# Performance work log

Measured on AMD Instinct MI355X. Metric: run time of the kernel, lower is better.

## Reference

```python
import jax, jax.numpy as jnp
import numpy as np

B, N, OUTERDIM, DIM, N_CLASSES = 2, 6000, 1024, 512, 2
HEADS, DIM_HEAD, INNER = 8, 64, 512
LANDMARKS, PINV_ITERS, KPAD = 256, 6, 16  # residual conv kernel 33 -> pad 16
SCALE = DIM_HEAD ** -0.5


def layer_norm(x, g, b, eps=1e-5):
    mu = x.mean(-1, keepdims=True)
    var = jnp.var(x, axis=-1, keepdims=True)
    return (x - mu) * jax.lax.rsqrt(var + eps) * g + b


def moore_penrose_pinv(x, iters=PINV_ITERS):
    # x: [b, h, m, m]
    abs_x = jnp.abs(x)
    col = abs_x.sum(-1)
    row = abs_x.sum(-2)
    z = jnp.swapaxes(x, -1, -2) / (jnp.max(col) * jnp.max(row))
    I = jnp.eye(x.shape[-1], dtype=x.dtype)
    for _ in range(iters):
        xz = x @ z
        z = 0.25 * z @ (13 * I - xz @ (15 * I - xz @ (7 * I - xz)))
    return z


def nystrom_attention(x, w_qkv, w_out, b_out, conv_w):
    b, n, _ = x.shape
    pad = (-n) % LANDMARKS
    xp = jnp.pad(x, ((0, 0), (pad, 0), (0, 0)))  # pad at FRONT, as in lucidrains impl
    npad = n + pad
    qkv = xp @ w_qkv.T  # [b, npad, 3*inner]
    q, k, v = [t.reshape(b, npad, HEADS, DIM_HEAD).transpose(0, 2, 1, 3)
               for t in jnp.split(qkv, 3, axis=-1)]
    q = q * SCALE
    l = npad // LANDMARKS  # tokens per landmark
    q_l = q.reshape(b, HEADS, LANDMARKS, l, DIM_HEAD).sum(3) / l
    k_l = k.reshape(b, HEADS, LANDMARKS, l, DIM_HEAD).sum(3) / l
    attn1 = jax.nn.softmax(jnp.einsum('bhid,bhjd->bhij', q, k_l), axis=-1)   # [b,h,npad,m]
    attn2 = jax.nn.softmax(jnp.einsum('bhid,bhjd->bhij', q_l, k_l), axis=-1)  # [b,h,m,m]
    attn3 = jax.nn.softmax(jnp.einsum('bhid,bhjd->bhij', q_l, k), axis=-1)    # [b,h,m,npad]
    out = (attn1 @ moore_penrose_pinv(attn2)) @ (attn3 @ v)  # [b,h,npad,d]
    # depthwise residual conv over sequence dim (per head), kernel (33,1)
    out = out + jax.lax.conv_general_dilated(
        v, conv_w, window_strides=(1, 1), padding=((KPAD, KPAD), (0, 0)),
        dimension_numbers=('NCHW', 'OIHW', 'NCHW'), feature_group_count=HEADS)
    out = out.transpose(0, 2, 1, 3).reshape(b, npad, INNER)
    out = out @ w_out.T + b_out
    return out[:, -n:]


def setup_inputs() -> dict:
    key = jax.random.key(0)
    ks = jax.random.split(key, 12)
    w = lambda k, shape: 0.02 * jax.random.normal(k, shape, dtype=jnp.float32)
    inp = {
        'data': jax.random.normal(ks[0], (B, N, OUTERDIM), dtype=jnp.float32),
        'w1': w(ks[1], (DIM, OUTERDIM)), 'b1': jnp.zeros((DIM,), jnp.float32),
        'cls_token': jax.random.normal(ks[2], (1, 1, DIM), dtype=jnp.float32),
        'ln1_g': jnp.ones((DIM,), jnp.float32), 'ln1_b': jnp.zeros((DIM,), jnp.float32),
        'qkv1_w': w(ks[3], (3 * INNER, DIM)),
        'out1_w': w(ks[4], (DIM, INNER)), 'out1_b': jnp.zeros((DIM,), jnp.float32),
        'conv1_w': w(ks[5], (HEADS, 1, 33, 1)),
        'ln2_g': jnp.ones((DIM,), jnp.float32), 'ln2_b': jnp.zeros((DIM,), jnp.float32),
        'qkv2_w': w(ks[6], (3 * INNER, DIM)),
        'out2_w': w(ks[7], (DIM, INNER)), 'out2_b': jnp.zeros((DIM,), jnp.float32),
        'conv2_w': w(ks[8], (HEADS, 1, 33, 1)),
        'lnf_g': jnp.ones((DIM,), jnp.float32), 'lnf_b': jnp.zeros((DIM,), jnp.float32),
        'w2': w(ks[9], (N_CLASSES, DIM)), 'b2': jnp.zeros((N_CLASSES,), jnp.float32),
    }
    return inp


def reference(data, w1, b1, cls_token, ln1_g, ln1_b, qkv1_w, out1_w, out1_b, conv1_w,
              ln2_g, ln2_b, qkv2_w, out2_w, out2_b, conv2_w, lnf_g, lnf_b, w2, b2):
    h = jax.nn.relu(data @ w1.T + b1)  # [B, N, DIM]
    H = h.shape[1]
    side = int(np.ceil(np.sqrt(H)))
    add = side * side - H
    h = jnp.concatenate([h, h[:, :add]], axis=1)  # square padding: 6084
    cls = jnp.broadcast_to(cls_token, (h.shape[0], 1, h.shape[2]))
    h = jnp.concatenate([cls, h], axis=1)  # +CLS: 6085
    h = h + nystrom_attention(layer_norm(h, ln1_g, ln1_b), qkv1_w, out1_w, out1_b, conv1_w)
    h = h + nystrom_attention(layer_norm(h, ln2_g, ln2_b), qkv2_w, out2_w, out2_b, conv2_w)
    h = layer_norm(h, lnf_g, lnf_b)[:, 0]
    logits = h @ w2.T + b2
    return logits
```

## Files before the change

### kernel.cpp

```cpp
#include <hip/hip_runtime.h>
#include <cstdint>
#include <cstddef>

namespace {

constexpr int DIMC  = 512;
constexpr int SEQ   = 6085;
constexpr int NPAD  = 6144;
constexpr int PADF  = 59;
constexpr int LMK   = 256;
constexpr int BHN   = 16;
constexpr int KSPL  = 16;
constexpr int MPADR = 6016;

typedef __attribute__((ext_vector_type(8))) short bf8_t;
typedef __attribute__((ext_vector_type(4))) float f4_t;

#define MFMA(a, b, c) __builtin_amdgcn_mfma_f32_16x16x32_bf16(a, b, c, 0, 0, 0)

#define SWZB(r, cu) (((((r) << 6) + ((cu) << 1))) ^ (((r) & 7) << 4))

#define GLDS16(gp, lp) __builtin_amdgcn_global_load_lds( \
    (const __attribute__((address_space(1))) void*)(gp), \
    (__attribute__((address_space(3))) void*)(lp), 16, 0, 0)

__device__ __forceinline__ ushort f2bf(float f) {
    union { float f; uint32_t u; } c{f};
    uint32_t u = c.u;
    return (ushort)((u + 0x7FFFu + ((u >> 16) & 1u)) >> 16);
}
__device__ __forceinline__ float bf2f(ushort u) {
    union { uint32_t u; float f; } c{(uint32_t)u << 16};
    return c.f;
}

__device__ __forceinline__ float waveSum(float v) {
#pragma unroll
    for (int o = 32; o > 0; o >>= 1) v += __shfl_xor(v, o, 64);
    return v;
}
__device__ __forceinline__ float waveMax(float v) {
#pragma unroll
    for (int o = 32; o > 0; o >>= 1) v = fmaxf(v, __shfl_xor(v, o, 64));
    return v;
}
__device__ __forceinline__ float blockSum256(float v, float* sm) {
    v = waveSum(v);
    __syncthreads();
    if ((threadIdx.x & 63) == 0) sm[threadIdx.x >> 6] = v;
    __syncthreads();
    return sm[0] + sm[1] + sm[2] + sm[3];
}
__device__ __forceinline__ float blockMax256(float v, float* sm) {
    v = waveMax(v);
    __syncthreads();
    if ((threadIdx.x & 63) == 0) sm[threadIdx.x >> 6] = v;
    __syncthreads();
    return fmaxf(fmaxf(sm[0], sm[1]), fmaxf(sm[2], sm[3]));
}
__device__ __forceinline__ float grpMax(float v) {
    v = fmaxf(v, __shfl_xor(v, 1, 64));
    v = fmaxf(v, __shfl_xor(v, 2, 64));
    v = fmaxf(v, __shfl_xor(v, 4, 64));
    v = fmaxf(v, __shfl_xor(v, 8, 64));
    return v;
}
__device__ __forceinline__ float grpSum(float v) {
    v += __shfl_xor(v, 1, 64);
    v += __shfl_xor(v, 2, 64);
    v += __shfl_xor(v, 4, 64);
    v += __shfl_xor(v, 8, 64);
    return v;
}

template<int EPI>
__global__ __launch_bounds__(256)
void gemm_bt(const ushort* __restrict__ A, const ushort* __restrict__ B,
             void* __restrict__ Cv, int M, int N, int K,
             int lda, int ldb, int ldc,
             long long sA, long long sB, long long sC,
             const float* __restrict__ bias, int relu,
             ushort* __restrict__ qp, ushort* __restrict__ kp, ushort* __restrict__ vp)
{
    __shared__ __align__(16) char As_s[128 * 128];
    __shared__ __align__(16) char Bs_s[128 * 128];
    const int z = blockIdx.z;
    const ushort* Ab = A + (size_t)z * sA;
    const ushort* Bb = B + (size_t)z * sB;
    const int row0 = blockIdx.y * 128, col0 = blockIdx.x * 128;
    const int tid = threadIdx.x, wid = tid >> 6, lane = tid & 63;
    const int wr = wid >> 1, wc = wid & 1, lr = lane & 15, kg = lane >> 4;
    const int srow = lane >> 3, sq = lane & 7;
    f4_t acc[4][4] = {};
    for (int k0 = 0; k0 < K; k0 += 64) {
        __syncthreads();
#pragma unroll
        for (int i = 0; i < 4; ++i) {
            int r = wid * 32 + i * 8 + srow;
            int qs = sq ^ (r & 7);
            GLDS16(Ab + (size_t)(row0 + r) * lda + k0 + qs * 8,
                   As_s + (wid * 32 + i * 8) * 128);
        }
#pragma unroll
        for (int i = 0; i < 4; ++i) {
            int r = wid * 32 + i * 8 + srow;
            int qs = sq ^ (r & 7);
            GLDS16(Bb + (size_t)(col0 + r) * ldb + k0 + qs * 8,
                   Bs_s + (wid * 32 + i * 8) * 128);
        }
        asm volatile("s_waitcnt vmcnt(0)" ::: "memory");
        __syncthreads();
#pragma unroll
        for (int ks = 0; ks < 2; ++ks) {
            bf8_t af[4], bg[4];
#pragma unroll
            for (int mr = 0; mr < 4; ++mr) {
                int r = wr * 64 + mr * 16 + lr;
                af[mr] = *(const bf8_t*)(As_s + r * 128 + ((((ks << 2) | kg) ^ (r & 7)) << 4));
            }
#pragma unroll
            for (int nr = 0; nr < 4; ++nr) {
                int r = wc * 64 + nr * 16 + lr;
                bg[nr] = *(const bf8_t*)(Bs_s + r * 128 + ((((ks << 2) | kg) ^ (r & 7)) << 4));
            }
#pragma unroll
            for (int mr = 0; mr < 4; ++mr)
#pragma unroll
                for (int nr = 0; nr < 4; ++nr)
                    acc[mr][nr] = MFMA(af[mr], bg[nr], acc[mr][nr]);
        }
    }
#pragma unroll
    for (int mr = 0; mr < 4; ++mr) {
#pragma unroll
        for (int nr = 0; nr < 4; ++nr) {
#pragma unroll
            for (int r = 0; r < 4; ++r) {
                int gm = row0 + wr * 64 + mr * 16 + kg * 4 + r;
                int gn = col0 + wc * 64 + nr * 16 + lr;
                if (gm >= M || gn >= N) continue;
                float val = acc[mr][nr][r];
                if (EPI == 0) {
                    if (bias) val += bias[gn];
                    if (relu) val = fmaxf(val, 0.f);
                    ((float*)Cv)[(size_t)z * sC + (size_t)gm * ldc + gn] = val;
                } else if (EPI == 1) {
                    ((ushort*)Cv)[(size_t)z * sC + (size_t)gm * ldc + gn] = f2bf(val);
                } else {
                    int b = (gm >= NPAD) ? 1 : 0;
                    int i = gm - b * NPAD;
                    int which = gn >> 9, hh = (gn >> 6) & 7, d = gn & 63;
                    if (which == 0)
                        qp[((size_t)(b * 8 + hh) * NPAD + i) * 64 + d] = f2bf(val * 0.125f);
                    else if (which == 1)
                        kp[((size_t)(b * 8 + hh) * NPAD + i) * 64 + d] = f2bf(val);
                    else
                        vp[((size_t)(b * 8 + hh) * 64 + d) * NPAD + i] = f2bf(val);
                }
            }
        }
    }
}

__global__ __launch_bounds__(256)
void pv_flash(const ushort* __restrict__ ql, const ushort* __restrict__ k,
              const ushort* __restrict__ vT, float* __restrict__ o2p,
              float* __restrict__ lmb, float* __restrict__ lsb)
{
    __shared__ __align__(16) char P_s[128 * 256];
    const int split = blockIdx.x, mt = blockIdx.y, bh = blockIdx.z;
    const int tid = threadIdx.x, wid = tid >> 6, lane = tid & 63;
    const int lr = lane & 15, kg = lane >> 4;
    const int rowb = wid * 32;
    const ushort* qlb = ql + ((size_t)bh * LMK + mt * 128) * 64;
    const ushort* kb  = k  + (size_t)bh * NPAD * 64;
    const ushort* vTb = vT + (size_t)bh * 64 * NPAD;
    const int kv0 = split * (NPAD / KSPL);

    float mrun[2][4], lrun[2][4];
    f4_t acco[2][4] = {};
#pragma unroll
    for (int mf = 0; mf < 2; ++mf)
#pragma unroll
        for (int r = 0; r < 4; ++r) { mrun[mf][r] = -3.0e38f; lrun[mf][r] = 0.f; }

    for (int kvt = 0; kvt < 3; ++kvt) {
        const int kvb = kv0 + kvt * 128;
        f4_t sacc[2][8] = {};
#pragma unroll
        for (int ks = 0; ks < 2; ++ks) {
            bf8_t af[2];
#pragma unroll
            for (int mf = 0; mf < 2; ++mf)
                af[mf] = *(const bf8_t*)&qlb[(size_t)(rowb + mf * 16 + lr) * 64 + ks * 32 + kg * 8];
#pragma unroll
            for (int nf = 0; nf < 8; ++nf) {
                bf8_t bg = *(const bf8_t*)&kb[(size_t)(kvb + nf * 16 + lr) * 64 + ks * 32 + kg * 8];
                sacc[0][nf] = MFMA(af[0], bg, sacc[0][nf]);
                sacc[1][nf] = MFMA(af[1], bg, sacc[1][nf]);
            }
        }
#pragma unroll
        for (int mf = 0; mf < 2; ++mf) {
            float tmax[4] = {-3.0e38f, -3.0e38f, -3.0e38f, -3.0e38f};
#pragma unroll
            for (int nf = 0; nf < 8; ++nf)
#pragma unroll
                for (int r = 0; r < 4; ++r) tmax[r] = fmaxf(tmax[r], sacc[mf][nf][r]);
#pragma unroll
            for (int r = 0; r < 4; ++r) {
                tmax[r] = grpMax(tmax[r]);
                float mnew = fmaxf(mrun[mf][r], tmax[r]);
                float sc = __expf(mrun[mf][r] - mnew);
                mrun[mf][r] = mnew;
                lrun[mf][r] *= sc;
#pragma unroll
                for (int nf2 = 0; nf2 < 4; ++nf2) acco[mf][nf2][r] *= sc;
            }
            float lsum[4] = {0.f, 0.f, 0.f, 0.f};
            const int rb2 = rowb + mf * 16 + kg * 4;
            const int cc2 = (lr & 7) * 2, chi = lr >> 3;
#pragma unroll
            for (int nf = 0; nf < 8; ++nf)
#pragma unroll
                for (int r = 0; r < 4; ++r) {
                    float e = __expf(sacc[mf][nf][r] - mrun[mf][r]);
                    lsum[r] += e;
                    int row = rb2 + r;
                    int chunk = (2 * nf + chi) ^ (row & 7);
                    *(ushort*)(P_s + row * 256 + chunk * 16 + cc2) = f2bf(e);
                }
#pragma unroll
            for (int r = 0; r < 4; ++r) lrun[mf][r] += grpSum(lsum[r]);
        }
#pragma unroll
        for (int kt2 = 0; kt2 < 4; ++kt2) {
            bf8_t af2[2];
#pragma unroll
            for (int mf = 0; mf < 2; ++mf) {
                int row = rowb + mf * 16 + lr;
                int chunk = (kt2 * 4 + kg) ^ (row & 7);
                af2[mf] = *(const bf8_t*)(P_s + row * 256 + chunk * 16);
            }
#pragma unroll
            for (int nf2 = 0; nf2 < 4; ++nf2) {
                bf8_t bg = *(const bf8_t*)&vTb[(size_t)(nf2 * 16 + lr) * NPAD + kvb + kt2 * 32 + kg * 8];
                acco[0][nf2] = MFMA(af2[0], bg, acco[0][nf2]);
                acco[1][nf2] = MFMA(af2[1], bg, acco[1][nf2]);
            }
        }
    }
#pragma unroll
    for (int mf = 0; mf < 2; ++mf)
#pragma unroll
        for (int nf2 = 0; nf2 < 4; ++nf2)
#pragma unroll
            for (int r = 0; r < 4; ++r) {
                int gm = mt * 128 + rowb + mf * 16 + kg * 4 + r;
                o2p[((size_t)(split * BHN + bh) * LMK + gm) * 64 + nf2 * 16 + lr] = acco[mf][nf2][r];
            }
    if (lr == 0) {
#pragma unroll
        for (int mf = 0; mf < 2; ++mf)
#pragma unroll
            for (int r = 0; r < 4; ++r) {
                int gm = mt * 128 + rowb + mf * 16 + kg * 4 + r;
                lmb[(size_t)(split * BHN + bh) * LMK + gm] = mrun[mf][r];
                lsb[(size_t)(split * BHN + bh) * LMK + gm] = lrun[mf][r];
            }
    }
}

__global__ void reduce_o2(const float* __restrict__ o2p, const float* __restrict__ lmb,
                          const float* __restrict__ lsb, ushort* __restrict__ o2)
{
    int idx = blockIdx.x * 256 + threadIdx.x;
    int bh = idx >> 14, m = (idx >> 6) & 255, d = idx & 63;
    float gm = -3.0e38f;
#pragma unroll
    for (int s = 0; s < KSPL; ++s)
        gm = fmaxf(gm, lmb[(size_t)(s * BHN + bh) * LMK + m]);
    float num = 0.f, den = 0.f;
#pragma unroll
    for (int s = 0; s < KSPL; ++s) {
        float wgt = __expf(lmb[(size_t)(s * BHN + bh) * LMK + m] - gm);
        num += wgt * o2p[((size_t)(s * BHN + bh) * LMK + m) * 64 + d];
        den += wgt * lsb[(size_t)(s * BHN + bh) * LMK + m];
    }
    o2[idx] = f2bf(num / den);
}

__global__ __launch_bounds__(256)
void attn1_fused(const ushort* __restrict__ q, const ushort* __restrict__ kl,
                 const ushort* __restrict__ Wt, ushort* __restrict__ ot)
{
    __shared__ __align__(16) char P_s[64 * 512];
    const int mt = blockIdx.x;
    const int bh = blockIdx.y;
    const int b = bh >> 3, hh = bh & 7;
    const int tid = threadIdx.x, wid = tid >> 6, lane = tid & 63;
    const int lr = lane & 15, kg = lane >> 4;
    const int row0 = mt * 64, rowb = wid * 16;
    const ushort* qb  = q  + (size_t)bh * NPAD * 64;
    const ushort* klb = kl + (size_t)bh * LMK * 64;
    const ushort* Wtb = Wt + (size_t)bh * 128 * 256;

    f4_t acc[16];
#pragma unroll
    for (int nf = 0; nf < 16; ++nf) acc[nf] = (f4_t){0.f, 0.f, 0.f, 0.f};
#pragma unroll
    for (int ks = 0; ks < 2; ++ks) {
        bf8_t af = *(const bf8_t*)&qb[(size_t)(row0 + rowb + lr) * 64 + ks * 32 + kg * 8];
#pragma unroll
        for (int nf = 0; nf < 16; ++nf) {
            bf8_t bg = *(const bf8_t*)&klb[(size_t)(nf * 16 + lr) * 64 + ks * 32 + kg * 8];
            acc[nf] = MFMA(af, bg, acc[nf]);
        }
    }
    float inv_s[4];
    {
        float mx[4] = {-3.0e38f, -3.0e38f, -3.0e38f, -3.0e38f};
#pragma unroll
        for (int nf = 0; nf < 16; ++nf)
#pragma unroll
            for (int r = 0; r < 4; ++r) mx[r] = fmaxf(mx[r], acc[nf][r]);
#pragma unroll
        for (int r = 0; r < 4; ++r) mx[r] = grpMax(mx[r]);
        float sum[4] = {0.f, 0.f, 0.f, 0.f};
        const int rb2 = rowb + kg * 4;
        const int cc2 = (lr & 7) * 2, chi = lr >> 3;
#pragma unroll
        for (int nf = 0; nf < 16; ++nf)
#pragma unroll
            for (int r = 0; r < 4; ++r) {
                float e = __expf(acc[nf][r] - mx[r]);
                sum[r] += e;
                int row = rb2 + r;
                int chunk = (2 * nf + chi) ^ (row & 7);
                *(ushort*)(P_s + row * 512 + chunk * 16 + cc2) = f2bf(e);
            }
#pragma unroll
        for (int r = 0; r < 4; ++r) inv_s[r] = 1.f / grpSum(sum[r]);
    }
    f4_t acc2[4] = {};
#pragma unroll
    for (int kt = 0; kt < 8; ++kt) {
        int row = rowb + lr;
        int chunk = (kt * 4 + kg) ^ (row & 7);
        bf8_t af2 = *(const bf8_t*)(P_s + row * 512 + chunk * 16);
#pragma unroll
        for (int nf = 0; nf < 4; ++nf) {
            bf8_t bg = *(const bf8_t*)&Wtb[(size_t)(nf * 16 + lr) * 256 + kt * 32 + kg * 8];
            acc2[nf] = MFMA(af2, bg, acc2[nf]);
        }
    }
#pragma unroll
    for (int nf = 0; nf < 4; ++nf)
#pragma unroll
        for (int r = 0; r < 4; ++r) {
            int gm = row0 + rowb + kg * 4 + r;
            int gn = nf * 16 + lr;
            ot[((size_t)(b * NPAD + gm)) * DIMC + hh * 64 + gn] = f2bf(acc2[nf][r] * inv_s[r]);
        }
}

__global__ __launch_bounds__(256)
void gemm_ns(const ushort* __restrict__ A, const ushort* __restrict__ B,
             ushort* __restrict__ C, ushort* __restrict__ C2, ushort* __restrict__ CT,
             float alpha, float c2d, int K, int N,
             long long sA, long long sB, long long sC, long long sCT)
{
    __shared__ __align__(16) char As_s[64 * 64];
    __shared__ __align__(16) char Bs_s[64 * 64];
    const int z = blockIdx.z;
    const int row0 = blockIdx.y * 64, col0 = blockIdx.x * 64;
    const int tid = threadIdx.x;
    const int wid = tid >> 6, lane = tid & 63;
    const int lr = lane & 15, kg = lane >> 4;
    const ushort* Ab = A + (size_t)z * sA;
    const ushort* Bb = B + (size_t)z * sB;
    f4_t acc[4] = {};
    const int am = tid >> 2, ac8 = (tid & 3) * 8;
    for (int k0 = 0; k0 < K; k0 += 32) {
        *(bf8_t*)(As_s + SWZB(am, ac8)) = *(const bf8_t*)&Ab[(size_t)(row0 + am) * K + k0 + ac8];
#pragma unroll
        for (int p = 0; p < 8; ++p) {
            int kk = p * 4 + (tid >> 6), n = tid & 63;
            *(ushort*)(Bs_s + SWZB(n, kk)) = Bb[(size_t)(k0 + kk) * N + col0 + n];
        }
        __syncthreads();
        bf8_t af = *(const bf8_t*)(As_s + SWZB(wid * 16 + lr, kg * 8));
#pragma unroll
        for (int j = 0; j < 4; ++j) {
            bf8_t bg = *(const bf8_t*)(Bs_s + SWZB(j * 16 + lr, kg * 8));
            acc[j] = MFMA(af, bg, acc[j]);
        }
        __syncthreads();
    }
#pragma unroll
    for (int j = 0; j < 4; ++j) {
#pragma unroll
        for (int r = 0; r < 4; ++r) {
            int gm = row0 + wid * 16 + kg * 4 + r;
            int gn = col0 + j * 16 + lr;
            float val = alpha * acc[j][r];
            if (C)  C[(size_t)z * sC + (size_t)gm * N + gn] = f2bf(val);
            if (C2) C2[(size_t)z * sC + (size_t)gm * N + gn] = f2bf(((gm == gn) ? c2d : 0.f) - val);
            if (CT) CT[(size_t)z * sCT + (size_t)gn * LMK + gm] = f2bf(val);
        }
    }
}

__global__ void cvt_bf16(const float* __restrict__ in, ushort* __restrict__ out, int n8) {
    int i = blockIdx.x * 256 + threadIdx.x;
    if (i >= n8) return;
    float4 a = ((const float4*)in)[i * 2], b = ((const float4*)in)[i * 2 + 1];
    ushort4 lo = { f2bf(a.x), f2bf(a.y), f2bf(a.z), f2bf(a.w) };
    ushort4 hi = { f2bf(b.x), f2bf(b.y), f2bf(b.z), f2bf(b.w) };
    ((ushort4*)out)[i * 2] = lo;
    ((ushort4*)out)[i * 2 + 1] = hi;
}

__global__ void extend_h(float* __restrict__ h, const float* __restrict__ cls) {
    int b = blockIdx.y, bx = blockIdx.x;
    float* hb = h + (size_t)b * SEQ * DIMC;
    for (int c = threadIdx.x; c < DIMC; c += 256) {
        if (bx == 0) hb[c] = cls[c];
        else hb[(size_t)(6000 + bx) * DIMC + c] = hb[(size_t)bx * DIMC + c];
    }
}

__global__ void zero_xp_pad(ushort* __restrict__ xp) {
    int e = blockIdx.x * 256 + threadIdx.x;
    int b = e / (PADF * DIMC);
    int rest = e - b * (PADF * DIMC);
    xp[(size_t)b * NPAD * DIMC + rest] = 0;
}

__global__ __launch_bounds__(128)
void ln_to_xp(const float* __restrict__ h, const float* __restrict__ g,
              const float* __restrict__ bb, ushort* __restrict__ xp)
{
    __shared__ float sm[2];
    int r = blockIdx.x;
    int b = r / SEQ, i = r - b * SEQ;
    int t = threadIdx.x;
    const float4* row = (const float4*)(h + (size_t)r * DIMC);
    float4 x = row[t];
    float s  = x.x + x.y + x.z + x.w;
    float sq = x.x * x.x + x.y * x.y + x.z * x.z + x.w * x.w;
    s = waveSum(s);
    sq = waveSum(sq);
    int w = t >> 6;
    if ((t & 63) == 0) sm[w] = s;
    __syncthreads();
    float S = sm[0] + sm[1];
    __syncthreads();
    if ((t & 63) == 0) sm[w] = sq;
    __syncthreads();
    float SQ = sm[0] + sm[1];
    float mu = S * (1.f / DIMC);
    float var = SQ * (1.f / DIMC) - mu * mu;
    float rs = rsqrtf(var + 1e-5f);
    float4 gg = ((const float4*)g)[t];
    float4 bv = ((const float4*)bb)[t];
    ushort4 o;
    o.x = f2bf((x.x - mu) * rs * gg.x + bv.x);
    o.y = f2bf((x.y - mu) * rs * gg.y + bv.y);
    o.z = f2bf((x.z - mu) * rs * gg.z + bv.z);
    o.w = f2bf((x.w - mu) * rs * gg.w + bv.w);
    ((ushort4*)(xp + ((size_t)b * NPAD + PADF + i) * DIMC))[t] = o;
}

__global__ void landmark_mean(const ushort* __restrict__ in, ushort* __restrict__ out) {
    int m = blockIdx.x, bh = blockIdx.y, d = threadIdx.x;
    const ushort* p = in + ((size_t)bh * NPAD + (size_t)m * (NPAD / LMK)) * 64 + d;
    float s = 0.f;
#pragma unroll
    for (int j = 0; j < NPAD / LMK; ++j) s += bf2f(p[(size_t)j * 64]);
    out[((size_t)bh * LMK + m) * 64 + d] = f2bf(s * (1.f / (NPAD / LMK)));
}

__global__ __launch_bounds__(256)
void softmax_bf256(ushort* __restrict__ S) {
    __shared__ float sm[4];
    ushort* p = S + (size_t)blockIdx.x * 256;
    int t = threadIdx.x;
    float v = bf2f(p[t]);
    float bm = blockMax256(v, sm);
    float e = __expf(v - bm);
    float bs = blockSum256(e, sm);
    p[t] = f2bf(e / bs);
}

__global__ __launch_bounds__(256)
void colsum_max(const ushort* __restrict__ X, float* __restrict__ scal) {
    __shared__ float sm[4];
    int bh = blockIdx.x, t = threadIdx.x;
    const ushort* Xb = X + ((size_t)bh << 16);
    float s = 0.f;
#pragma unroll 8
    for (int i = 0; i < 256; ++i) s += bf2f(Xb[(size_t)i * 256 + t]);
    float m = blockMax256(s, sm);
    if (t == 0) atomicMax((unsigned int*)scal, __float_as_uint(m));
}

__global__ void init_z(const ushort* __restrict__ X, const float* __restrict__ scal,
                       ushort* __restrict__ Z) {
    size_t e = (size_t)blockIdx.x * 256 + threadIdx.x;
    int c = (int)(e & 255);
    int r = (int)((e >> 8) & 255);
    size_t bh = e >> 16;
    float inv = 1.f / scal[0];
    Z[e] = f2bf(bf2f(X[(bh << 16) + (size_t)c * 256 + r]) * inv);
}

__global__ __launch_bounds__(256)
void conv_add(const ushort* __restrict__ vT, const float* __restrict__ cw,
              ushort* __restrict__ ot)
{
    __shared__ float w[33];
    __shared__ ushort vt[64][97];
    int bh = blockIdx.y;
    int b = bh >> 3, hh = bh & 7;
    int i0 = blockIdx.x * 64;
    int t = threadIdx.x;
    if (t < 33) w[t] = cw[hh * 33 + t];
    const ushort* vTb = vT + (size_t)bh * 64 * NPAD;
    for (int idx = t; idx < 64 * 96; idx += 256) {
        int d = idx / 96, jj = idx - d * 96;
        int j = i0 - 16 + jj;
        vt[d][jj] = (j >= 0 && j < NPAD) ? vTb[(size_t)d * NPAD + j] : (ushort)0;
    }
    __syncthreads();
    int d = t & 63;
    for (int ii = t >> 6; ii < 64; ii += 4) {
        float acc = 0.f;
#pragma unroll
        for (int kk = 0; kk < 33; ++kk) acc += w[kk] * bf2f(vt[d][ii + kk]);
        size_t off = ((size_t)(b * NPAD + i0 + ii)) * DIMC + hh * 64 + d;
        ot[off] = f2bf(bf2f(ot[off]) + acc);
    }
}

__global__ void residual_add(float* __restrict__ h, const float* __restrict__ y) {
    size_t e = (size_t)blockIdx.x * 256 + threadIdx.x;
    int c = (int)(e & 511);
    size_t ri = e >> 9;
    int i = (int)(ri % SEQ);
    int b = (int)(ri / SEQ);
    h[e] += y[((size_t)b * NPAD + PADF + i) * DIMC + c];
}

__global__ __launch_bounds__(256)
void final_head(const float* __restrict__ h, const float* __restrict__ g,
                const float* __restrict__ bb, const float* __restrict__ w2,
                const float* __restrict__ b2, float* __restrict__ out)
{
    __shared__ float row[DIMC];
    __shared__ float sm[4];
    int b = blockIdx.x;
    int t = threadIdx.x;
    const float* x = h + (size_t)b * SEQ * DIMC;
    float v0 = x[t], v1 = x[t + 256];
    float S = blockSum256(v0 + v1, sm);
    float SQ = blockSum256(v0 * v0 + v1 * v1, sm);
    float mu = S * (1.f / DIMC);
    float rs = rsqrtf(SQ * (1.f / DIMC) - mu * mu + 1e-5f);
    row[t] = (v0 - mu) * rs * g[t] + bb[t];
    row[t + 256] = (v1 - mu) * rs * g[t + 256] + bb[t + 256];
    __syncthreads();
    if (t < 64) {
        float a0 = 0.f, a1 = 0.f;
        for (int idx = t; idx < DIMC; idx += 64) {
            a0 += row[idx] * w2[idx];
            a1 += row[idx] * w2[DIMC + idx];
        }
        a0 = waveSum(a0);
        a1 = waveSum(a1);
        if (t == 0) {
            out[b * 2 + 0] = a0 + b2[0];
            out[b * 2 + 1] = a1 + b2[1];
        }
    }
}

void bt(int epi, const ushort* A, const ushort* B, void* C, int M, int N, int K,
        int lda, int ldb, int ldc, long long sA, long long sB, long long sC, int batch,
        const float* bias, int relu, ushort* qp, ushort* kp, ushort* vp, hipStream_t s)
{
    dim3 g((N + 127) / 128, (M + 127) / 128, batch), blk(256);
    switch (epi) {
    case 0: gemm_bt<0><<<g, blk, 0, s>>>(A, B, C, M, N, K, lda, ldb, ldc, sA, sB, sC, bias, relu, qp, kp, vp); break;
    case 1: gemm_bt<1><<<g, blk, 0, s>>>(A, B, C, M, N, K, lda, ldb, ldc, sA, sB, sC, bias, relu, qp, kp, vp); break;
    default: gemm_bt<2><<<g, blk, 0, s>>>(A, B, C, M, N, K, lda, ldb, ldc, sA, sB, sC, bias, relu, qp, kp, vp); break;
    }
}

void ns(const ushort* A, const ushort* B, ushort* C, ushort* C2, ushort* CT,
        float alpha, float c2d, int M, int N, int K,
        long long sA, long long sB, long long sC, long long sCT, hipStream_t s)
{
    dim3 g(N / 64, M / 64, BHN), blk(256);
    gemm_ns<<<g, blk, 0, s>>>(A, B, C, C2, CT, alpha, c2d, K, N, sA, sB, sC, sCT);
}

struct WS {
    float *h, *scal, *o2p, *y, *lmb, *lsb;
    ushort *xp, *q, *k, *vT, *ql, *kl;
    ushort *datab, *w1b, *qkvwb1, *qkvwb2, *outwb1, *outwb2;
    ushort *X, *Z0, *Z1, *XZ, *TA, *TB, *TC;
    ushort *o2b, *Wt, *S, *ot;
};

void nystrom_layer(float* h, const float* lng, const float* lnb,
                   const ushort* qkvwb, const ushort* outwb, const float* outb,
                   const float* convw, const WS& w, hipStream_t s)
{
    const long long SM = (long long)LMK * LMK;
    zero_xp_pad<<<(2 * PADF * DIMC) / 256, 256, 0, s>>>(w.xp);
    ln_to_xp<<<2 * SEQ, 128, 0, s>>>(h, lng, lnb, w.xp);
    bt(2, w.xp, qkvwb, nullptr, 2 * NPAD, 3 * DIMC, DIMC, DIMC, DIMC, 0,
       0, 0, 0, 1, nullptr, 0, w.q, w.k, w.vT, s);
    landmark_mean<<<dim3(LMK, BHN), 64, 0, s>>>(w.q, w.ql);
    landmark_mean<<<dim3(LMK, BHN), 64, 0, s>>>(w.k, w.kl);
    bt(1, w.ql, w.kl, w.X, LMK, LMK, 64, 64, 64, LMK,
       (long long)LMK * 64, (long long)LMK * 64, SM, BHN, nullptr, 0, nullptr, nullptr, nullptr, s);
    softmax_bf256<<<BHN * LMK, 256, 0, s>>>(w.X);
    hipMemsetAsync(w.scal, 0, 8, s);
    colsum_max<<<BHN, 256, 0, s>>>(w.X, w.scal);
    init_z<<<(BHN * LMK * LMK) / 256, 256, 0, s>>>(w.X, w.scal, w.Z0);
    ushort* Zc = w.Z0;
    ushort* Zn = w.Z1;
    for (int it = 0; it < 6; ++it) {
        ns(w.X, Zc, w.XZ, w.TA, nullptr, 1.f, 7.f, LMK, LMK, LMK, SM, SM, SM, 0, s);
        ns(w.XZ, w.TA, w.TB, w.TC, nullptr, 1.f, 15.f, LMK, LMK, LMK, SM, SM, SM, 0, s);
        ns(w.XZ, w.TC, w.TB, w.TA, nullptr, 1.f, 13.f, LMK, LMK, LMK, SM, SM, SM, 0, s);
        ns(Zc, w.TA, Zn, nullptr, nullptr, 0.25f, 0.f, LMK, LMK, LMK, SM, SM, SM, 0, s);
        ushort* t = Zc; Zc = Zn; Zn = t;
    }
    pv_flash<<<dim3(KSPL, 2, BHN), 256, 0, s>>>(w.ql, w.k, w.vT, w.o2p, w.lmb, w.lsb);
    reduce_o2<<<BHN * LMK * 64 / 256, 256, 0, s>>>(w.o2p, w.lmb, w.lsb, w.o2b);
    ns(Zc, w.o2b, nullptr, nullptr, w.Wt, 1.f, 0.f, LMK, 64, LMK,
       SM, (long long)LMK * 64, 0, 128 * 256, s);
    attn1_fused<<<dim3(NPAD / 64, BHN), 256, 0, s>>>(w.q, w.kl, w.Wt, w.ot);
    conv_add<<<dim3(NPAD / 64, BHN), 256, 0, s>>>(w.vT, convw, w.ot);
    bt(0, w.ot, outwb, w.y, 2 * NPAD, DIMC, DIMC, DIMC, DIMC, DIMC,
       0, 0, 0, 1, outb, 0, nullptr, nullptr, nullptr, s);
    residual_add<<<(2 * SEQ * DIMC) / 256, 256, 0, s>>>(h, w.y);
}

}

extern "C" void kernel_launch(void* const* d_in, const int* in_sizes, int n_in,
                              void* d_out, int out_size, void* d_ws, size_t ws_size,
                              hipStream_t stream)
{
    (void)in_sizes; (void)n_in; (void)out_size;
    const float* data  = (const float*)d_in[0];
    const float* w1    = (const float*)d_in[1];
    const float* b1    = (const float*)d_in[2];
    const float* cls   = (const float*)d_in[3];
    const float* ln1g  = (const float*)d_in[4];
    const float* ln1b  = (const float*)d_in[5];
    const float* qkv1w = (const float*)d_in[6];
    const float* out1w = (const float*)d_in[7];
    const float* out1b = (const float*)d_in[8];
    const float* conv1 = (const float*)d_in[9];
    const float* ln2g  = (const float*)d_in[10];
    const float* ln2b  = (const float*)d_in[11];
    const float* qkv2w = (const float*)d_in[12];
    const float* out2w = (const float*)d_in[13];
    const float* out2b = (const float*)d_in[14];
    const float* conv2 = (const float*)d_in[15];
    const float* lnfg  = (const float*)d_in[16];
    const float* lnfb  = (const float*)d_in[17];
    const float* w2    = (const float*)d_in[18];
    const float* b2    = (const float*)d_in[19];
    float* out = (float*)d_out;

    if (ws_size < 209473792ull) return;
    char* p = (char*)d_ws;
    auto alloc = [&](size_t bytes) { char* r = p; p += (bytes + 255) & ~(size_t)255; return r; };
    WS w;
    w.h     = (float*)alloc((size_t)2 * SEQ * DIMC * 4);
    w.xp    = (ushort*)alloc((size_t)2 * NPAD * DIMC * 2);
    w.q     = (ushort*)alloc((size_t)BHN * NPAD * 64 * 2);
    w.k     = (ushort*)alloc((size_t)BHN * NPAD * 64 * 2);
    w.vT    = (ushort*)alloc((size_t)BHN * 64 * NPAD * 2);
    w.ql    = (ushort*)alloc((size_t)BHN * LMK * 64 * 2);
    w.kl    = (ushort*)alloc((size_t)BHN * LMK * 64 * 2);
    w.scal  = (float*)alloc(256);
    w.datab = (ushort*)alloc((size_t)2 * MPADR * 1024 * 2);
    w.w1b   = (ushort*)alloc((size_t)512 * 1024 * 2);
    w.qkvwb1= (ushort*)alloc((size_t)1536 * 512 * 2);
    w.qkvwb2= (ushort*)alloc((size_t)1536 * 512 * 2);
    w.outwb1= (ushort*)alloc((size_t)512 * 512 * 2);
    w.outwb2= (ushort*)alloc((size_t)512 * 512 * 2);
    w.X     = (ushort*)alloc((size_t)BHN * LMK * LMK * 2);
    w.Z0    = (ushort*)alloc((size_t)BHN * LMK * LMK * 2);
    w.Z1    = (ushort*)alloc((size_t)BHN * LMK * LMK * 2);
    w.XZ    = (ushort*)alloc((size_t)BHN * LMK * LMK * 2);
    w.TA    = (ushort*)alloc((size_t)BHN * LMK * LMK * 2);
    w.TB    = (ushort*)alloc((size_t)BHN * LMK * LMK * 2);
    w.TC    = (ushort*)alloc((size_t)BHN * LMK * LMK * 2);
    w.o2p   = (float*)alloc((size_t)KSPL * BHN * LMK * 64 * 4);
    w.lmb   = (float*)alloc((size_t)KSPL * BHN * LMK * 4);
    w.lsb   = (float*)alloc((size_t)KSPL * BHN * LMK * 4);
    w.o2b   = (ushort*)alloc((size_t)BHN * LMK * 64 * 2);
    w.Wt    = (ushort*)alloc((size_t)BHN * 128 * 256 * 2);
    w.S     = (ushort*)alloc((size_t)BHN * LMK * NPAD * 2);
    w.y     = (float*)w.S;
    w.ot    = w.k;

    for (int b = 0; b < 2; ++b)
        cvt_bf16<<<3000, 256, 0, stream>>>(data + (size_t)b * 6000 * 1024,
                                           w.datab + (size_t)b * MPADR * 1024, 768000);
    cvt_bf16<<<256, 256, 0, stream>>>(w1, w.w1b, 65536);
    cvt_bf16<<<384, 256, 0, stream>>>(qkv1w, w.qkvwb1, 98304);
    cvt_bf16<<<384, 256, 0, stream>>>(qkv2w, w.qkvwb2, 98304);
    cvt_bf16<<<128, 256, 0, stream>>>(out1w, w.outwb1, 32768);
    cvt_bf16<<<128, 256, 0, stream>>>(out2w, w.outwb2, 32768);

    bt(0, w.datab, w.w1b, w.h + DIMC, 6000, DIMC, 1024, 1024, 1024, DIMC,
       (long long)MPADR * 1024, 0, (long long)SEQ * DIMC, 2, b1, 1,
       nullptr, nullptr, nullptr, stream);
    extend_h<<<dim3(85, 2), 256, 0, stream>>>(w.h, cls);

    nystrom_layer(w.h, ln1g, ln1b, w.qkvwb1, w.outwb1, out1b, conv1, w, stream);
    nystrom_layer(w.h, ln2g, ln2b, w.qkvwb2, w.outwb2, out2b, conv2, w, stream);

    final_head<<<2, 256, 0, stream>>>(w.h, lnfg, lnfb, w2, b2, out);
}
```

Measured before the change: 1.094 ms.

## Fuse residual depthwise conv into attn1 kernel and widen pv_flash split count

Removes the separate conv_add kernel: the QKV GEMM epilogue now also writes V in row-major layout, and attn1_fused stages a 96-row V window in shared memory and adds the 33-tap depthwise conv before its bf16 store. This avoids re-reading and re-writing the attention output. pv_flash now processes a single 128-token KV tile per block (KSPL raised to 48) with no online rescaling, giving more parallel blocks, while reduce_o2 merges three times as many partials. The extra V copy adds a write in the GEMM epilogue, and the y buffer is aliased onto the enlarged o2p buffer.

Result: slower. 1.131 ms (+3.4%).

```diff
diff --git a/kernel.cpp b/kernel.cpp
--- a/kernel.cpp
+++ b/kernel.cpp
@@ -10,7 +10,7 @@
 constexpr int PADF  = 59;
 constexpr int LMK   = 256;
 constexpr int BHN   = 16;
-constexpr int KSPL  = 16;
+constexpr int KSPL  = 48;
 constexpr int MPADR = 6016;
 
 typedef __attribute__((ext_vector_type(8))) short bf8_t;
@@ -80,7 +80,8 @@
              int lda, int ldb, int ldc,
              long long sA, long long sB, long long sC,
              const float* __restrict__ bias, int relu,
-             ushort* __restrict__ qp, ushort* __restrict__ kp, ushort* __restrict__ vp)
+             ushort* __restrict__ qp, ushort* __restrict__ kp,
+             ushort* __restrict__ vp, ushort* __restrict__ vtp)
 {
     __shared__ __align__(16) char As_s[128 * 128];
     __shared__ __align__(16) char Bs_s[128 * 128];
@@ -150,12 +151,16 @@
                     int b = (gm >= NPAD) ? 1 : 0;
                     int i = gm - b * NPAD;
                     int which = gn >> 9, hh = (gn >> 6) & 7, d = gn & 63;
+                    int bh = b * 8 + hh;
                     if (which == 0)
-                        qp[((size_t)(b * 8 + hh) * NPAD + i) * 64 + d] = f2bf(val * 0.125f);
+                        qp[((size_t)bh * NPAD + i) * 64 + d] = f2bf(val * 0.125f);
                     else if (which == 1)
-                        kp[((size_t)(b * 8 + hh) * NPAD + i) * 64 + d] = f2bf(val);
-                    else
-                        vp[((size_t)(b * 8 + hh) * 64 + d) * NPAD + i] = f2bf(val);
+                        kp[((size_t)bh * NPAD + i) * 64 + d] = f2bf(val);
+                    else {
+                        ushort bv = f2bf(val);
+                        vp[((size_t)bh * NPAD + i) * 64 + d] = bv;
+                        vtp[((size_t)bh * 64 + d) * NPAD + i] = bv;
+                    }
                 }
             }
         }
@@ -175,79 +180,63 @@
     const ushort* qlb = ql + ((size_t)bh * LMK + mt * 128) * 64;
     const ushort* kb  = k  + (size_t)bh * NPAD * 64;
     const ushort* vTb = vT + (size_t)bh * 64 * NPAD;
-    const int kv0 = split * (NPAD / KSPL);
-
-    float mrun[2][4], lrun[2][4];
+    const int kvb = split * 128;
+
+    f4_t sacc[2][8] = {};
+#pragma unroll
+    for (int ks = 0; ks < 2; ++ks) {
+        bf8_t af[2];
+#pragma unroll
+        for (int mf = 0; mf < 2; ++mf)
+            af[mf] = *(const bf8_t*)&qlb[(size_t)(rowb + mf * 16 + lr) * 64 + ks * 32 + kg * 8];
+#pragma unroll
+        for (int nf = 0; nf < 8; ++nf) {
+            bf8_t bg = *(const bf8_t*)&kb[(size_t)(kvb + nf * 16 + lr) * 64 + ks * 32 + kg * 8];
+            sacc[0][nf] = MFMA(af[0], bg, sacc[0][nf]);
+            sacc[1][nf] = MFMA(af[1], bg, sacc[1][nf]);
+        }
+    }
+    float mloc[2][4], lloc[2][4];
+#pragma unroll
+    for (int mf = 0; mf < 2; ++mf) {
+        float tmax[4] = {-3.0e38f, -3.0e38f, -3.0e38f, -3.0e38f};
+#pragma unroll
+        for (int nf = 0; nf < 8; ++nf)
+#pragma unroll
+            for (int r = 0; r < 4; ++r) tmax[r] = fmaxf(tmax[r], sacc[mf][nf][r]);
+#pragma unroll
+        for (int r = 0; r < 4; ++r) { tmax[r] = grpMax(tmax[r]); mloc[mf][r] = tmax[r]; }
+        float lsum[4] = {0.f, 0.f, 0.f, 0.f};
+        const int rb2 = rowb + mf * 16 + kg * 4;
+        const int cc2 = (lr & 7) * 2, chi = lr >> 3;
+#pragma unroll
+        for (int nf = 0; nf < 8; ++nf)
+#pragma unroll
+            for (int r = 0; r < 4; ++r) {
+                float e = __expf(sacc[mf][nf][r] - tmax[r]);
+                lsum[r] += e;
+                int row = rb2 + r;
+                int chunk = (2 * nf + chi) ^ (row & 7);
+                *(ushort*)(P_s + row * 256 + chunk * 16 + cc2) = f2bf(e);
+            }
+#pragma unroll
+        for (int r = 0; r < 4; ++r) lloc[mf][r] = grpSum(lsum[r]);
+    }
     f4_t acco[2][4] = {};
 #pragma unroll
-    for (int mf = 0; mf < 2; ++mf)
-#pragma unroll
-        for (int r = 0; r < 4; ++r) { mrun[mf][r] = -3.0e38f; lrun[mf][r] = 0.f; }
-
-    for (int kvt = 0; kvt < 3; ++kvt) {
-        const int kvb = kv0 + kvt * 128;
-        f4_t sacc[2][8] = {};
-#pragma unroll
-        for (int ks = 0; ks < 2; ++ks) {
-            bf8_t af[2];
-#pragma unroll
-            for (int mf = 0; mf < 2; ++mf)
-                af[mf] = *(const bf8_t*)&qlb[(size_t)(rowb + mf * 16 + lr) * 64 + ks * 32 + kg * 8];
-#pragma unroll
-            for (int nf = 0; nf < 8; ++nf) {
-                bf8_t bg = *(const bf8_t*)&kb[(size_t)(kvb + nf * 16 + lr) * 64 + ks * 32 + kg * 8];
-                sacc[0][nf] = MFMA(af[0], bg, sacc[0][nf]);
-                sacc[1][nf] = MFMA(af[1], bg, sacc[1][nf]);
-            }
-        }
+    for (int kt2 = 0; kt2 < 4; ++kt2) {
+        bf8_t af2[2];
 #pragma unroll
         for (int mf = 0; mf < 2; ++mf) {
-            float tmax[4] = {-3.0e38f, -3.0e38f, -3.0e38f, -3.0e38f};
-#pragma unroll
-            for (int nf = 0; nf < 8; ++nf)
-#pragma unroll
-                for (int r = 0; r < 4; ++r) tmax[r] = fmaxf(tmax[r], sacc[mf][nf][r]);
-#pragma unroll
-            for (int r = 0; r < 4; ++r) {
-                tmax[r] = grpMax(tmax[r]);
-                float mnew = fmaxf(mrun[mf][r], tmax[r]);
-                float sc = __expf(mrun[mf][r] - mnew);
-                mrun[mf][r] = mnew;
-                lrun[mf][r] *= sc;
-#pragma unroll
-                for (int nf2 = 0; nf2 < 4; ++nf2) acco[mf][nf2][r] *= sc;
-            }
-            float lsum[4] = {0.f, 0.f, 0.f, 0.f};
-            const int rb2 = rowb + mf * 16 + kg * 4;
-            const int cc2 = (lr & 7) * 2, chi = lr >> 3;
-#pragma unroll
-            for (int nf = 0; nf < 8; ++nf)
-#pragma unroll
-                for (int r = 0; r < 4; ++r) {
-                    float e = __expf(sacc[mf][nf][r] - mrun[mf][r]);
-                    lsum[r] += e;
-                    int row = rb2 + r;
-                    int chunk = (2 * nf + chi) ^ (row & 7);
-                    *(ushort*)(P_s + row * 256 + chunk * 16 + cc2) = f2bf(e);
-                }
-#pragma unroll
-            for (int r = 0; r < 4; ++r) lrun[mf][r] += grpSum(lsum[r]);
-        }
-#pragma unroll
-        for (int kt2 = 0; kt2 < 4; ++kt2) {
-            bf8_t af2[2];
-#pragma unroll
-            for (int mf = 0; mf < 2; ++mf) {
-                int row = rowb + mf * 16 + lr;
-                int chunk = (kt2 * 4 + kg) ^ (row & 7);
-                af2[mf] = *(const bf8_t*)(P_s + row * 256 + chunk * 16);
-            }
-#pragma unroll
-            for (int nf2 = 0; nf2 < 4; ++nf2) {
-                bf8_t bg = *(const bf8_t*)&vTb[(size_t)(nf2 * 16 + lr) * NPAD + kvb + kt2 * 32 + kg * 8];
-                acco[0][nf2] = MFMA(af2[0], bg, acco[0][nf2]);
-                acco[1][nf2] = MFMA(af2[1], bg, acco[1][nf2]);
-            }
+            int row = rowb + mf * 16 + lr;
+            int chunk = (kt2 * 4 + kg) ^ (row & 7);
+            af2[mf] = *(const bf8_t*)(P_s + row * 256 + chunk * 16);
+        }
+#pragma unroll
+        for (int nf2 = 0; nf2 < 4; ++nf2) {
+            bf8_t bg = *(const bf8_t*)&vTb[(size_t)(nf2 * 16 + lr) * NPAD + kvb + kt2 * 32 + kg * 8];
+            acco[0][nf2] = MFMA(af2[0], bg, acco[0][nf2]);
+            acco[1][nf2] = MFMA(af2[1], bg, acco[1][nf2]);
         }
     }
 #pragma unroll
@@ -265,8 +254,8 @@
 #pragma unroll
             for (int r = 0; r < 4; ++r) {
                 int gm = mt * 128 + rowb + mf * 16 + kg * 4 + r;
-                lmb[(size_t)(split * BHN + bh) * LMK + gm] = mrun[mf][r];
-                lsb[(size_t)(split * BHN + bh) * LMK + gm] = lrun[mf][r];
+                lmb[(size_t)(split * BHN + bh) * LMK + gm] = mloc[mf][r];
+                lsb[(size_t)(split * BHN + bh) * LMK + gm] = lloc[mf][r];
             }
     }
 }
@@ -277,14 +266,14 @@
     int idx = blockIdx.x * 256 + threadIdx.x;
     int bh = idx >> 14, m = (idx >> 6) & 255, d = idx & 63;
     float gm = -3.0e38f;
-#pragma unroll
+#pragma unroll 8
     for (int s = 0; s < KSPL; ++s)
         gm = fmaxf(gm, lmb[(size_t)(s * BHN + bh) * LMK + m]);
     float num = 0.f, den = 0.f;
-#pragma unroll
+#pragma unroll 4
     for (int s = 0; s < KSPL; ++s) {
         float wgt = __expf(lmb[(size_t)(s * BHN + bh) * LMK + m] - gm);
-        num += wgt * o2p[((size_t)(s * BHN + bh) * LMK + m) * 64 + d];
+        num += wgt * o2p[((size_t)(s * BHN + bh) << 14) + (m << 6) + d];
         den += wgt * lsb[(size_t)(s * BHN + bh) * LMK + m];
     }
     o2[idx] = f2bf(num / den);
@@ -292,9 +281,12 @@
 
 __global__ __launch_bounds__(256)
 void attn1_fused(const ushort* __restrict__ q, const ushort* __restrict__ kl,
-                 const ushort* __restrict__ Wt, ushort* __restrict__ ot)
+                 const ushort* __restrict__ Wt, const ushort* __restrict__ v,
+                 const float* __restrict__ cw, ushort* __restrict__ ot)
 {
     __shared__ __align__(16) char P_s[64 * 512];
+    __shared__ ushort vt[96][65];
+    __shared__ float wsm[33];
     const int mt = blockIdx.x;
     const int bh = blockIdx.y;
     const int b = bh >> 3, hh = bh & 7;
@@ -304,6 +296,15 @@
     const ushort* qb  = q  + (size_t)bh * NPAD * 64;
     const ushort* klb = kl + (size_t)bh * LMK * 64;
     const ushort* Wtb = Wt + (size_t)bh * 128 * 256;
+    const ushort* vb  = v  + (size_t)bh * NPAD * 64;
+
+    if (tid < 33) wsm[tid] = cw[hh * 33 + tid];
+    for (int idx = tid; idx < 96 * 64; idx += 256) {
+        int rr = idx >> 6, d = idx & 63;
+        int j = row0 - 16 + rr;
+        vt[rr][d] = (j >= 0 && j < NPAD) ? vb[(size_t)j * 64 + d] : (ushort)0;
+    }
+    __syncthreads();
 
     f4_t acc[16];
 #pragma unroll
@@ -355,13 +356,20 @@
         }
     }
 #pragma unroll
-    for (int nf = 0; nf < 4; ++nf)
+    for (int nf = 0; nf < 4; ++nf) {
+        int gn = nf * 16 + lr;
 #pragma unroll
         for (int r = 0; r < 4; ++r) {
-            int gm = row0 + rowb + kg * 4 + r;
-            int gn = nf * 16 + lr;
-            ot[((size_t)(b * NPAD + gm)) * DIMC + hh * 64 + gn] = f2bf(acc2[nf][r] * inv_s[r]);
-        }
+            int lm = rowb + kg * 4 + r;
+            float cv = 0.f;
+#pragma unroll
+            for (int kk = 0; kk < 33; ++kk)
+                cv += wsm[kk] * bf2f(vt[lm + kk][gn]);
+            int gm = row0 + lm;
+            ot[((size_t)(b * NPAD + gm)) * DIMC + hh * 64 + gn] =
+                f2bf(acc2[nf][r] * inv_s[r] + cv);
+        }
+    }
 }
 
 __global__ __launch_bounds__(256)
@@ -515,34 +523,6 @@
     Z[e] = f2bf(bf2f(X[(bh << 16) + (size_t)c * 256 + r]) * inv);
 }
 
-__global__ __launch_bounds__(256)
-void conv_add(const ushort* __restrict__ vT, const float* __restrict__ cw,
-              ushort* __restrict__ ot)
-{
-    __shared__ float w[33];
-    __shared__ ushort vt[64][97];
-    int bh = blockIdx.y;
-    int b = bh >> 3, hh = bh & 7;
-    int i0 = blockIdx.x * 64;
-    int t = threadIdx.x;
-    if (t < 33) w[t] = cw[hh * 33 + t];
-    const ushort* vTb = vT + (size_t)bh * 64 * NPAD;
-    for (int idx = t; idx < 64 * 96; idx += 256) {
-        int d = idx / 96, jj = idx - d * 96;
-        int j = i0 - 16 + jj;
-        vt[d][jj] = (j >= 0 && j < NPAD) ? vTb[(size_t)d * NPAD + j] : (ushort)0;
-    }
-    __syncthreads();
-    int d = t & 63;
-    for (int ii = t >> 6; ii < 64; ii += 4) {
-        float acc = 0.f;
-#pragma unroll
-        for (int kk = 0; kk < 33; ++kk) acc += w[kk] * bf2f(vt[d][ii + kk]);
-        size_t off = ((size_t)(b * NPAD + i0 + ii)) * DIMC + hh * 64 + d;
-        ot[off] = f2bf(bf2f(ot[off]) + acc);
-    }
-}
-
 __global__ void residual_add(float* __restrict__ h, const float* __restrict__ y) {
     size_t e = (size_t)blockIdx.x * 256 + threadIdx.x;
     int c = (int)(e & 511);
@@ -587,13 +567,14 @@
 
 void bt(int epi, const ushort* A, const ushort* B, void* C, int M, int N, int K,
         int lda, int ldb, int ldc, long long sA, long long sB, long long sC, int batch,
-        const float* bias, int relu, ushort* qp, ushort* kp, ushort* vp, hipStream_t s)
+        const float* bias, int relu, ushort* qp, ushort* kp, ushort* vp, ushort* vtp,
+        hipStream_t s)
 {
     dim3 g((N + 127) / 128, (M + 127) / 128, batch), blk(256);
     switch (epi) {
-    case 0: gemm_bt<0><<<g, blk, 0, s>>>(A, B, C, M, N, K, lda, ldb, ldc, sA, sB, sC, bias, relu, qp, kp, vp); break;
-    case 1: gemm_bt<1><<<g, blk, 0, s>>>(A, B, C, M, N, K, lda, ldb, ldc, sA, sB, sC, bias, relu, qp, kp, vp); break;
-    default: gemm_bt<2><<<g, blk, 0, s>>>(A, B, C, M, N, K, lda, ldb, ldc, sA, sB, sC, bias, relu, qp, kp, vp); break;
+    case 0: gemm_bt<0><<<g, blk, 0, s>>>(A, B, C, M, N, K, lda, ldb, ldc, sA, sB, sC, bias, relu, qp, kp, vp, vtp); break;
+    case 1: gemm_bt<1><<<g, blk, 0, s>>>(A, B, C, M, N, K, lda, ldb, ldc, sA, sB, sC, bias, relu, qp, kp, vp, vtp); break;
+    default: gemm_bt<2><<<g, blk, 0, s>>>(A, B, C, M, N, K, lda, ldb, ldc, sA, sB, sC, bias, relu, qp, kp, vp, vtp); break;
     }
 }
 
@@ -607,10 +588,10 @@
 
 struct WS {
     float *h, *scal, *o2p, *y, *lmb, *lsb;
-    ushort *xp, *q, *k, *vT, *ql, *kl;
+    ushort *xp, *q, *k, *v, *vT, *ql, *kl;
     ushort *datab, *w1b, *qkvwb1, *qkvwb2, *outwb1, *outwb2;
     ushort *X, *Z0, *Z1, *XZ, *TA, *TB, *TC;
-    ushort *o2b, *Wt, *S, *ot;
+    ushort *o2b, *Wt, *ot;
 };
 
 void nystrom_layer(float* h, const float* lng, const float* lnb,
@@ -621,11 +602,12 @@
     zero_xp_pad<<<(2 * PADF * DIMC) / 256, 256, 0, s>>>(w.xp);
     ln_to_xp<<<2 * SEQ, 128, 0, s>>>(h, lng, lnb, w.xp);
     bt(2, w.xp, qkvwb, nullptr, 2 * NPAD, 3 * DIMC, DIMC, DIMC, DIMC, 0,
-       0, 0, 0, 1, nullptr, 0, w.q, w.k, w.vT, s);
+       0, 0, 0, 1, nullptr, 0, w.q, w.k, w.v, w.vT, s);
     landmark_mean<<<dim3(LMK, BHN), 64, 0, s>>>(w.q, w.ql);
     landmark_mean<<<dim3(LMK, BHN), 64, 0, s>>>(w.k, w.kl);
     bt(1, w.ql, w.kl, w.X, LMK, LMK, 64, 64, 64, LMK,
-       (long long)LMK * 64, (long long)LMK * 64, SM, BHN, nullptr, 0, nullptr, nullptr, nullptr, s);
+       (long long)LMK * 64, (long long)LMK * 64, SM, BHN,
+       nullptr, 0, nullptr, nullptr, nullptr, nullptr, s);
     softmax_bf256<<<BHN * LMK, 256, 0, s>>>(w.X);
     hipMemsetAsync(w.scal, 0, 8, s);
     colsum_max<<<BHN, 256, 0, s>>>(w.X, w.scal);
@@ -643,10 +625,9 @@
     reduce_o2<<<BHN * LMK * 64 / 256, 256, 0, s>>>(w.o2p, w.lmb, w.lsb, w.o2b);
     ns(Zc, w.o2b, nullptr, nullptr, w.Wt, 1.f, 0.f, LMK, 64, LMK,
        SM, (long long)LMK * 64, 0, 128 * 256, s);
-    attn1_fused<<<dim3(NPAD / 64, BHN), 256, 0, s>>>(w.q, w.kl, w.Wt, w.ot);
-    conv_add<<<dim3(NPAD / 64, BHN), 256, 0, s>>>(w.vT, convw, w.ot);
+    attn1_fused<<<dim3(NPAD / 64, BHN), 256, 0, s>>>(w.q, w.kl, w.Wt, w.v, convw, w.ot);
     bt(0, w.ot, outwb, w.y, 2 * NPAD, DIMC, DIMC, DIMC, DIMC, DIMC,
-       0, 0, 0, 1, outb, 0, nullptr, nullptr, nullptr, s);
+       0, 0, 0, 1, outb, 0, nullptr, nullptr, nullptr, nullptr, s);
     residual_add<<<(2 * SEQ * DIMC) / 256, 256, 0, s>>>(h, w.y);
 }
 
@@ -687,6 +668,7 @@
     w.xp    = (ushort*)alloc((size_t)2 * NPAD * DIMC * 2);
     w.q     = (ushort*)alloc((size_t)BHN * NPAD * 64 * 2);
     w.k     = (ushort*)alloc((size_t)BHN * NPAD * 64 * 2);
+    w.v     = (ushort*)alloc((size_t)BHN * NPAD * 64 * 2);
     w.vT    = (ushort*)alloc((size_t)BHN * 64 * NPAD * 2);
     w.ql    = (ushort*)alloc((size_t)BHN * LMK * 64 * 2);
     w.kl    = (ushort*)alloc((size_t)BHN * LMK * 64 * 2);
@@ -709,8 +691,7 @@
     w.lsb   = (float*)alloc((size_t)KSPL * BHN * LMK * 4);
     w.o2b   = (ushort*)alloc((size_t)BHN * LMK * 64 * 2);
     w.Wt    = (ushort*)alloc((size_t)BHN * 128 * 256 * 2);
-    w.S     = (ushort*)alloc((size_t)BHN * LMK * NPAD * 2);
-    w.y     = (float*)w.S;
+    w.y     = (float*)w.o2p;
     w.ot    = w.k;
 
     for (int b = 0; b < 2; ++b)
@@ -724,7 +705,7 @@
 
     bt(0, w.datab, w.w1b, w.h + DIMC, 6000, DIMC, 1024, 1024, 1024, DIMC,
        (long long)MPADR * 1024, 0, (long long)SEQ * DIMC, 2, b1, 1,
-       nullptr, nullptr, nullptr, stream);
+       nullptr, nullptr, nullptr, nullptr, stream);
     extend_h<<<dim3(85, 2), 256, 0, stream>>>(w.h, cls);
 
     nystrom_layer(w.h, ln1g, ln1b, w.qkvwb1, w.outwb1, out1b, conv1, w, stream);
```
